# Kernel tuning notes

Hardware: AMD Instinct MI355X
Metric: run time of the kernel (lower is better)

The kernel has to match this reference:

```python
import jax, jax.numpy as jnp
import numpy as np

NEG = -1000000000.0  # mask fill value from the original code


def setup_inputs() -> dict:
    key = jax.random.key(0)
    k1, k2, k3 = jax.random.split(key, 3)
    B, L, H, E = 2, 2048, 16, 64
    S, D = L, E
    queries = jax.random.normal(k1, (B, L, H, E), dtype=jnp.float32)
    keys = jax.random.normal(k2, (B, S, H, E), dtype=jnp.float32)
    values = jax.random.normal(k3, (B, S, H, D), dtype=jnp.float32)
    return {"queries": queries, "keys": keys, "values": values}


def reference(queries, keys, values):
    B, L, H, E = queries.shape
    S = keys.shape[1]
    scale = 1.0 / np.sqrt(E)
    # scores: [B, H, L, S]
    scores = jnp.einsum('blhe,bshe->bhls', queries, keys)
    # Faithful to original: tf.where(band_part(ones,-1,0), -1e9, scores)
    # i.e. fill -1e9 where the LOWER triangle (incl. diagonal) is True.
    tril = jnp.tril(jnp.ones((L, S), dtype=bool))  # [L, S]
    scores = jnp.where(tril[None, None, :, :], jnp.float32(NEG), scores)
    # scale applied AFTER masking, as in the original
    A = jax.nn.softmax(scale * scores, axis=-1)
    # dropout is identity at inference
    V = jnp.einsum('bhls,bshd->blhd', A, values)
    return V
```

## Files before the change

kernel.cpp:

```cpp
#include <hip/hip_runtime.h>


#define B_ 2
#define L_ 2048
#define H_ 16
#define E_ 64
#define S_ 2048
#define D_ 64
#define NR_ 16
#define QSCALE 0.18033688011112042f

typedef __attribute__((ext_vector_type(4))) float f32x4;
typedef __attribute__((ext_vector_type(16))) float f32x16;
typedef __attribute__((ext_vector_type(8))) short short8;
typedef __attribute__((ext_vector_type(2))) unsigned int uint2v;
typedef __attribute__((ext_vector_type(4))) unsigned int uint4v;
typedef unsigned short ushort;

__device__ __forceinline__ unsigned short f2bf(float f) {
  unsigned int u = __builtin_bit_cast(unsigned int, f);
  u = (u + 0x7FFFu + ((u >> 16) & 1u)) >> 16;
  return (unsigned short)u;
}
__device__ __forceinline__ unsigned int pkbf(float a, float b) {
  return (unsigned int)f2bf(a) | ((unsigned int)f2bf(b) << 16);
}
__device__ __forceinline__ unsigned cvtpk(float a, float b) {
  unsigned r;
  asm("v_cvt_pk_bf16_f32 %0, %1, %2" : "=v"(r) : "v"(a), "v"(b));
  return r;
}
__device__ __forceinline__ uint2v plswap(unsigned a, unsigned b, int hi) {
#if __has_builtin(__builtin_amdgcn_permlane32_swap)
  (void)hi;
  return __builtin_amdgcn_permlane32_swap(a, b, false, false);
#else
  unsigned ax = (unsigned)__shfl_xor((int)a, 32);
  unsigned bx = (unsigned)__shfl_xor((int)b, 32);
  uint2v r;
  r[0] = hi ? bx : a;
  r[1] = hi ? b : ax;
  return r;
#endif
}
__device__ __forceinline__ f32x16 zero16() {
  f32x16 z;
#pragma unroll
  for (int i = 0; i < 16; ++i) z[i] = 0.f;
  return z;
}

__global__ __launch_bounds__(256) void prep_all(const float* __restrict__ Kg,
                                                const float* __restrict__ Vg,
                                                ushort* __restrict__ Kb,
                                                ushort* __restrict__ Vt) {
  __shared__ ushort Tl[64][72];
  const int blk = (int)blockIdx.x;
  const int tid = (int)threadIdx.x;
  if (blk < 2048) {
    const int t = blk * 256 + tid;
    const int orow = t >> 3, e0 = (t & 7) << 3;
    const int s = orow & (S_ - 1), bh = orow >> 11;
    const int b = bh >> 4, h = bh & 15;
    const float* src = Kg + ((size_t)((b * S_ + s) * H_ + h)) * E_ + e0;
    f32x4 a = ((const f32x4*)src)[0], c = ((const f32x4*)src)[1];
    short8 o;
    o[0]=(short)f2bf(a[0]); o[1]=(short)f2bf(a[1]); o[2]=(short)f2bf(a[2]); o[3]=(short)f2bf(a[3]);
    o[4]=(short)f2bf(c[0]); o[5]=(short)f2bf(c[1]); o[6]=(short)f2bf(c[2]); o[7]=(short)f2bf(c[3]);
    *(short8*)(Kb + (size_t)orow * E_ + e0) = o;
  } else {
    const int vb = blk - 2048;
    const int bh = vb & 31, st = vb >> 5;
    const int b = bh >> 4, h = bh & 15;
    const int s0 = st << 6;
    {
      const int sr = tid >> 2, d0 = (tid & 3) << 4;
      const float* src = Vg + ((size_t)((b * S_ + s0 + sr) * H_ + h)) * D_ + d0;
      f32x4 v0 = ((const f32x4*)src)[0], v1 = ((const f32x4*)src)[1];
      f32x4 v2 = ((const f32x4*)src)[2], v3 = ((const f32x4*)src)[3];
      ushort* dst = &Tl[sr][d0];
      dst[0]=f2bf(v0[0]); dst[1]=f2bf(v0[1]); dst[2]=f2bf(v0[2]); dst[3]=f2bf(v0[3]);
      dst[4]=f2bf(v1[0]); dst[5]=f2bf(v1[1]); dst[6]=f2bf(v1[2]); dst[7]=f2bf(v1[3]);
      dst[8]=f2bf(v2[0]); dst[9]=f2bf(v2[1]); dst[10]=f2bf(v2[2]); dst[11]=f2bf(v2[3]);
      dst[12]=f2bf(v3[0]); dst[13]=f2bf(v3[1]); dst[14]=f2bf(v3[2]); dst[15]=f2bf(v3[3]);
    }
    __syncthreads();
    {
      const int d = tid >> 2, sb = (tid & 3) << 4;
      short8 o0, o1;
#pragma unroll
      for (int j = 0; j < 8; ++j) {
        o0[j] = (short)Tl[sb + j][d];
        o1[j] = (short)Tl[sb + 8 + j][d];
      }
      ushort* dst = Vt + ((size_t)bh * D_ + d) * S_ + s0 + sb;
      *(short8*)dst = o0;
      *(short8*)(dst + 8) = o1;
    }
  }
}

struct Stage8 { short8 k[4]; short8 v[4]; };

__device__ __forceinline__ Stage8 sload(const ushort* __restrict__ Kbh,
                                        const ushort* __restrict__ VbhT,
                                        int s0, int tid) {
  Stage8 r;
  const int sl = tid >> 1, gb = (tid & 1) * 4;
  const ushort* kp = Kbh + (size_t)(s0 + sl) * E_ + gb * 8;
  r.k[0] = *(const short8*)(kp);
  r.k[1] = *(const short8*)(kp + 8);
  r.k[2] = *(const short8*)(kp + 16);
  r.k[3] = *(const short8*)(kp + 24);
  const int d = tid >> 2, sb = (tid & 3) * 32;
  const ushort* vp = VbhT + (size_t)d * S_ + s0 + sb;
  r.v[0] = *(const short8*)(vp);
  r.v[1] = *(const short8*)(vp + 8);
  r.v[2] = *(const short8*)(vp + 16);
  r.v[3] = *(const short8*)(vp + 24);
  return r;
}

__device__ __forceinline__ void swrite(ushort* SM, const Stage8& r, int tid) {
  const int sl = tid >> 1, gb = (tid & 1) * 4;
#pragma unroll
  for (int j = 0; j < 4; ++j)
    *(short8*)(SM + sl * 64 + (((gb + j) ^ (sl & 7)) << 3)) = r.k[j];
  const int d = tid >> 2, sgb = (tid & 3) * 4;
#pragma unroll
  for (int j = 0; j < 4; ++j) {
    const int sgg = sgb + j;
    *(short8*)(SM + 8192 + (sgg >> 3) * 4096 + d * 64 + (((sgg & 7) ^ (d & 7)) << 3)) = r.v[j];
  }
}

__global__ __launch_bounds__(256, 2) void attn_fwd9(
    const float* __restrict__ Qg, const ushort* __restrict__ Kb,
    const ushort* __restrict__ Vt, float* __restrict__ Og) {
  const int bh = (int)blockIdx.x;
  const int b = bh >> 4, h = bh & 15;
  const int yi0 = (int)blockIdx.y;
  const int yi = (yi0 < 8) ? yi0 : 23 - yi0;
  const int q0 = yi << 7;
  const int tid = (int)threadIdx.x;
  const int w = tid >> 6, lane = tid & 63;
  const int hi = lane >> 5, c32 = lane & 31;
  const int qbase = q0 + (w << 5);
  const int qrow = qbase + c32;

  __shared__ __align__(16) ushort SM[2][16384];

  const ushort* Kbh = Kb + (size_t)bh * (S_ * E_);
  const ushort* VbhT = Vt + (size_t)bh * (D_ * S_);

  short8 qf[4];
  {
    const float* qr = Qg + ((size_t)((b * L_ + qrow) * H_ + h)) * E_;
#pragma unroll
    for (int kc = 0; kc < 4; ++kc) {
      f32x4 x = *(const f32x4*)(qr + kc * 16 + hi * 8);
      f32x4 y = *(const f32x4*)(qr + kc * 16 + hi * 8 + 4);
      short8 q;
      q[0]=(short)f2bf(QSCALE*x[0]); q[1]=(short)f2bf(QSCALE*x[1]);
      q[2]=(short)f2bf(QSCALE*x[2]); q[3]=(short)f2bf(QSCALE*x[3]);
      q[4]=(short)f2bf(QSCALE*y[0]); q[5]=(short)f2bf(QSCALE*y[1]);
      q[6]=(short)f2bf(QSCALE*y[2]); q[7]=(short)f2bf(QSCALE*y[3]);
      qf[kc] = q;
    }
  }

  f32x16 acc0 = zero16(), acc1 = zero16();
  float m_run = -1e30f, dsum = 0.f;

  const int r0 = (q0 + 1) >> 7;

  {
    Stage8 s = sload(Kbh, VbhT, r0 << 7, tid);
    swrite(SM[0], s, tid);
  }
  __syncthreads();

  for (int r = r0; r < NR_; ++r) {
    const int cur = (r - r0) & 1;
    const bool more = (r + 1) < NR_;
    Stage8 nxt;
    if (more) nxt = sload(Kbh, VbhT, (r + 1) << 7, tid);

    const ushort* img = SM[cur];
#pragma unroll
    for (int half = 0; half < 2; ++half) {
      const int s0 = (r << 7) + (half << 6);
      if (s0 + 63 > qbase) {
        f32x16 st0 = zero16(), st1 = zero16();
        __builtin_amdgcn_s_setprio(1);
#pragma unroll
        for (int kc = 0; kc < 4; ++kc) {
          const int gg = 2 * kc + hi;
          const int rl0 = (half << 6) + c32, rl1 = rl0 + 32;
          short8 k0 = *(const short8*)(img + rl0 * 64 + ((gg ^ (rl0 & 7)) << 3));
          short8 k1 = *(const short8*)(img + rl1 * 64 + ((gg ^ (rl1 & 7)) << 3));
          st0 = __builtin_amdgcn_mfma_f32_32x32x16_bf16(k0, qf[kc], st0, 0, 0, 0);
          st1 = __builtin_amdgcn_mfma_f32_32x32x16_bf16(k1, qf[kc], st1, 0, 0, 0);
        }
        __builtin_amdgcn_s_setprio(0);

        if (s0 < qbase + 32) {
#pragma unroll
          for (int r16 = 0; r16 < 16; ++r16) {
            const int ko = (r16 & 3) + 8 * (r16 >> 2) + 4 * hi;
            st0[r16] = (s0 + ko <= qrow) ? -1e30f : st0[r16];
            st1[r16] = (s0 + 32 + ko <= qrow) ? -1e30f : st1[r16];
          }
        }

        float pmax = -1e30f;
#pragma unroll
        for (int r16 = 0; r16 < 16; ++r16) pmax = fmaxf(pmax, fmaxf(st0[r16], st1[r16]));
        if (__any(pmax > m_run + 8.0f)) {
          float rm = fmaxf(pmax, __shfl_xor(pmax, 32));
          float m_new = fmaxf(m_run, rm);
          float alpha = exp2f(m_run - m_new);
          dsum *= alpha;
#pragma unroll
          for (int r16 = 0; r16 < 16; ++r16) {
            float ar = __shfl(alpha, (r16 & 3) + 8 * (r16 >> 2) + 4 * hi);
            acc0[r16] *= ar;
            acc1[r16] *= ar;
          }
          m_run = m_new;
        }

        float ps = 0.f;
#pragma unroll
        for (int r16 = 0; r16 < 16; ++r16) { st0[r16] = exp2f(st0[r16] - m_run); ps += st0[r16]; }
#pragma unroll
        for (int r16 = 0; r16 < 16; ++r16) { st1[r16] = exp2f(st1[r16] - m_run); ps += st1[r16]; }
        dsum += ps;

        short8 pf[4];
#pragma unroll
        for (int kp = 0; kp < 4; ++kp) {
          const f32x16 stt = (kp < 2) ? st0 : st1;
          const int u = kp & 1;
          unsigned pA0 = cvtpk(stt[8 * u + 0], stt[8 * u + 1]);
          unsigned pA1 = cvtpk(stt[8 * u + 2], stt[8 * u + 3]);
          unsigned pB0 = cvtpk(stt[8 * u + 4], stt[8 * u + 5]);
          unsigned pB1 = cvtpk(stt[8 * u + 6], stt[8 * u + 7]);
          uint2v sw0 = plswap(pA0, pB0, hi);
          uint2v sw1 = plswap(pA1, pB1, hi);
          uint4v fv;
          fv[0] = sw0[0]; fv[1] = sw1[0]; fv[2] = sw0[1]; fv[3] = sw1[1];
          pf[kp] = __builtin_bit_cast(short8, fv);
        }

        __builtin_amdgcn_s_setprio(1);
#pragma unroll
        for (int kp = 0; kp < 4; ++kp) {
          const int sg = 2 * kp + hi;
          const ushort* vb = img + 8192 + half * 4096;
          short8 v0 = *(const short8*)(vb + c32 * 64 + ((sg ^ (c32 & 7)) << 3));
          short8 v1 = *(const short8*)(vb + (32 + c32) * 64 + ((sg ^ (c32 & 7)) << 3));
          acc0 = __builtin_amdgcn_mfma_f32_32x32x16_bf16(pf[kp], v0, acc0, 0, 0, 0);
          acc1 = __builtin_amdgcn_mfma_f32_32x32x16_bf16(pf[kp], v1, acc1, 0, 0, 0);
        }
        __builtin_amdgcn_s_setprio(0);
      }
    }

    if (more) swrite(SM[cur ^ 1], nxt, tid);
    __syncthreads();
  }

  float dfull = dsum + __shfl_xor(dsum, 32);
#pragma unroll
  for (int r16 = 0; r16 < 16; ++r16) {
    const int row = (r16 & 3) + 8 * (r16 >> 2) + 4 * hi;
    const float dn = __shfl(dfull, row);
    const int grow = qbase + row;
    if (grow != L_ - 1) {
      const float inv = 1.0f / dn;
      const size_t base = ((size_t)((b * L_ + grow) * H_ + h)) * D_;
      Og[base + c32] = acc0[r16] * inv;
      Og[base + 32 + c32] = acc1[r16] * inv;
    }
  }
}

__global__ __launch_bounds__(256) void vmean_part(const float* __restrict__ Vg,
                                                  float* __restrict__ ws) {
  const int g = blockIdx.x;
  const int slab = g & 15, bh = g >> 4;
  const int b = bh >> 4, h = bh & 15;
  const int lane = (int)threadIdx.x & 63, w = (int)threadIdx.x >> 6;
  const int s0 = (slab << 7) + (w << 5);
  const float* base = Vg + ((size_t)((b * S_ + s0) * H_ + h)) * D_ + lane;
  float sum = 0.f;
#pragma unroll 4
  for (int i = 0; i < 32; ++i) sum += base[(size_t)i * (H_ * D_)];
  __shared__ float red[4][64];
  red[w][lane] = sum;
  __syncthreads();
  if (w == 0)
    ws[(size_t)g * 64 + lane] =
        red[0][lane] + red[1][lane] + red[2][lane] + red[3][lane];
}

__global__ __launch_bounds__(64) void vmean_comb(const float* __restrict__ ws,
                                                 float* __restrict__ Og) {
  const int bh = blockIdx.x;
  const int b = bh >> 4, h = bh & 15;
  const int lane = (int)threadIdx.x;
  float t = 0.f;
#pragma unroll
  for (int i = 0; i < 16; ++i) t += ws[(size_t)(bh * 16 + i) * 64 + lane];
  Og[((size_t)((b * L_ + (L_ - 1)) * H_ + h)) * D_ + lane] = t * (1.0f / (float)S_);
}

__global__ __launch_bounds__(256) void attn_fwd(
    const float* __restrict__ Qg, const float* __restrict__ Kg,
    const float* __restrict__ Vg, float* __restrict__ Og) {
  const int bh = blockIdx.x;
  const int b = bh >> 4, h = bh & 15;
  const int q0 = blockIdx.y << 6;
  const int tid = (int)threadIdx.x;
  const int lane = tid & 63;
  const int w = tid >> 6;
  const int gp = lane >> 4;
  const int c = lane & 15;
  const int qbase = q0 + (w << 4);

  __shared__ unsigned short Kl[32][72];
  __shared__ unsigned short Vts[64][40];

  short8 qf0, qf1;
  {
    const float* qrow = Qg + ((size_t)((b * L_ + (qbase + c)) * H_ + h)) * E_;
    const f32x4* q0p = (const f32x4*)(qrow + (gp << 3));
    const f32x4* q1p = (const f32x4*)(qrow + 32 + (gp << 3));
    f32x4 a0 = q0p[0], b0 = q0p[1], a1 = q1p[0], b1 = q1p[1];
    float t0[8] = {a0[0],a0[1],a0[2],a0[3],b0[0],b0[1],b0[2],b0[3]};
    float t1[8] = {a1[0],a1[1],a1[2],a1[3],b1[0],b1[1],b1[2],b1[3]};
#pragma unroll
    for (int j = 0; j < 8; ++j) {
      qf0[j] = (short)f2bf(0.125f * t0[j]);
      qf1[j] = (short)f2bf(0.125f * t1[j]);
    }
  }

  f32x4 accO[4];
#pragma unroll
  for (int k0 = 0; k0 < 4; ++k0) accO[k0] = (f32x4){0.f, 0.f, 0.f, 0.f};
  float m_run = -1e30f, denom = 0.f;

  const int c0 = (q0 + 1) >> 5;
  const int srow = tid >> 3;
  const int scol = (tid & 7) << 3;

  for (int ch = c0; ch < (S_ >> 5); ++ch) {
    const int s0 = ch << 5;
    __syncthreads();
    {
      const size_t rbase = ((size_t)((b * S_ + (s0 + srow)) * H_ + h));
      const float* kp = Kg + rbase * E_ + scol;
      f32x4 ka = *(const f32x4*)kp;
      f32x4 kb = *(const f32x4*)(kp + 4);
      short8 kv;
      kv[0]=(short)f2bf(ka[0]); kv[1]=(short)f2bf(ka[1]);
      kv[2]=(short)f2bf(ka[2]); kv[3]=(short)f2bf(ka[3]);
      kv[4]=(short)f2bf(kb[0]); kv[5]=(short)f2bf(kb[1]);
      kv[6]=(short)f2bf(kb[2]); kv[7]=(short)f2bf(kb[3]);
      *(short8*)&Kl[srow][scol] = kv;
      const float* vp = Vg + rbase * D_ + scol;
      f32x4 va = *(const f32x4*)vp;
      f32x4 vb = *(const f32x4*)(vp + 4);
      Vts[scol + 0][srow] = f2bf(va[0]);
      Vts[scol + 1][srow] = f2bf(va[1]);
      Vts[scol + 2][srow] = f2bf(va[2]);
      Vts[scol + 3][srow] = f2bf(va[3]);
      Vts[scol + 4][srow] = f2bf(vb[0]);
      Vts[scol + 5][srow] = f2bf(vb[1]);
      Vts[scol + 6][srow] = f2bf(vb[2]);
      Vts[scol + 7][srow] = f2bf(vb[3]);
    }
    __syncthreads();
    if (s0 + 31 <= qbase) continue;

    f32x4 st0 = {0.f,0.f,0.f,0.f}, st1 = {0.f,0.f,0.f,0.f};
    {
      short8 kf;
      kf = *(const short8*)&Kl[c][(gp << 3)];
      st0 = __builtin_amdgcn_mfma_f32_16x16x32_bf16(kf, qf0, st0, 0, 0, 0);
      kf = *(const short8*)&Kl[c][32 + (gp << 3)];
      st0 = __builtin_amdgcn_mfma_f32_16x16x32_bf16(kf, qf1, st0, 0, 0, 0);
      kf = *(const short8*)&Kl[16 + c][(gp << 3)];
      st1 = __builtin_amdgcn_mfma_f32_16x16x32_bf16(kf, qf0, st1, 0, 0, 0);
      kf = *(const short8*)&Kl[16 + c][32 + (gp << 3)];
      st1 = __builtin_amdgcn_mfma_f32_16x16x32_bf16(kf, qf1, st1, 0, 0, 0);
    }

    const int lrow = qbase + c;
    float p[8];
    {
      float sarr[8] = {st0[0], st0[1], st0[2], st0[3], st1[0], st1[1], st1[2], st1[3]};
      float mx = -1e30f;
#pragma unroll
      for (int i = 0; i < 8; ++i) {
        int sg = s0 + ((i >> 2) << 4) + (gp << 2) + (i & 3);
        float v = (sg > lrow) ? sarr[i] : -1e30f;
        p[i] = v;
        mx = fmaxf(mx, v);
      }
      mx = fmaxf(mx, __shfl_xor(mx, 16));
      mx = fmaxf(mx, __shfl_xor(mx, 32));
      float m_new = fmaxf(m_run, mx);
      float sum = 0.f;
#pragma unroll
      for (int i = 0; i < 8; ++i) { p[i] = __expf(p[i] - m_new); sum += p[i]; }
      sum += __shfl_xor(sum, 16);
      sum += __shfl_xor(sum, 32);
      float alpha = __expf(m_run - m_new);
      m_run = m_new;
      denom = denom * alpha + sum;
      float ar0 = __shfl(alpha, (gp << 2) + 0);
      float ar1 = __shfl(alpha, (gp << 2) + 1);
      float ar2 = __shfl(alpha, (gp << 2) + 2);
      float ar3 = __shfl(alpha, (gp << 2) + 3);
#pragma unroll
      for (int k0 = 0; k0 < 4; ++k0) {
        accO[k0][0] *= ar0; accO[k0][1] *= ar1;
        accO[k0][2] *= ar2; accO[k0][3] *= ar3;
      }
    }

    {
      unsigned int pA0 = pkbf(p[0], p[1]), pA1 = pkbf(p[2], p[3]);
      unsigned int pB0 = pkbf(p[4], p[5]), pB1 = pkbf(p[6], p[7]);
      const int al = (gp << 1) & 3;
      const int src0 = (al << 4) + c, src1 = src0 + 16;
      unsigned int a0 = (unsigned int)__shfl((int)pA0, src0);
      unsigned int a1 = (unsigned int)__shfl((int)pA1, src0);
      unsigned int a2 = (unsigned int)__shfl((int)pA0, src1);
      unsigned int a3 = (unsigned int)__shfl((int)pA1, src1);
      unsigned int b0 = (unsigned int)__shfl((int)pB0, src0);
      unsigned int b1 = (unsigned int)__shfl((int)pB1, src0);
      unsigned int b2 = (unsigned int)__shfl((int)pB0, src1);
      unsigned int b3 = (unsigned int)__shfl((int)pB1, src1);
      const bool useA = (gp < 2);
      uint4v fv;
      fv[0] = useA ? a0 : b0;
      fv[1] = useA ? a1 : b1;
      fv[2] = useA ? a2 : b2;
      fv[3] = useA ? a3 : b3;
      short8 pfv = __builtin_bit_cast(short8, fv);
#pragma unroll
      for (int k0 = 0; k0 < 4; ++k0) {
        short8 vf = *(const short8*)&Vts[(k0 << 4) + c][(gp << 3)];
        accO[k0] = __builtin_amdgcn_mfma_f32_16x16x32_bf16(pfv, vf, accO[k0], 0, 0, 0);
      }
    }
  }

  float dr[4];
  dr[0] = __shfl(denom, (gp << 2) + 0);
  dr[1] = __shfl(denom, (gp << 2) + 1);
  dr[2] = __shfl(denom, (gp << 2) + 2);
  dr[3] = __shfl(denom, (gp << 2) + 3);
#pragma unroll
  for (int r = 0; r < 4; ++r) {
    const int grow = qbase + (gp << 2) + r;
    if (grow == L_ - 1) continue;
    const size_t base = ((size_t)((b * L_ + grow) * H_ + h)) * D_ + c;
    const float inv = 1.0f / dr[r];
    Og[base +  0] = accO[0][r] * inv;
    Og[base + 16] = accO[1][r] * inv;
    Og[base + 32] = accO[2][r] * inv;
    Og[base + 48] = accO[3][r] * inv;
  }
}

__global__ __launch_bounds__(256) void vmean_fix(const float* __restrict__ Vg,
                                                 float* __restrict__ Og) {
  const int bh = blockIdx.x;
  const int b = bh >> 4, h = bh & 15;
  const int t = (int)threadIdx.x;
  const int lane = t & 63, w = t >> 6;
  float sum = 0.f;
  for (int s = w; s < S_; s += 4)
    sum += Vg[((size_t)((b * S_ + s) * H_ + h)) * D_ + lane];
  __shared__ float red[4][64];
  red[w][lane] = sum;
  __syncthreads();
  if (w == 0) {
    float tot = red[0][lane] + red[1][lane] + red[2][lane] + red[3][lane];
    Og[((size_t)((b * L_ + (L_ - 1)) * H_ + h)) * D_ + lane] = tot * (1.0f / (float)S_);
  }
}

extern "C" void kernel_launch(void* const* d_in, const int* in_sizes, int n_in,
                              void* d_out, int out_size, void* d_ws, size_t ws_size,
                              hipStream_t stream) {
  const float* Q = (const float*)d_in[0];
  const float* K = (const float*)d_in[1];
  const float* V = (const float*)d_in[2];
  float* O = (float*)d_out;
  const size_t szK = (size_t)B_ * H_ * S_ * E_ * 2;
  const size_t szV = (size_t)B_ * H_ * D_ * S_ * 2;
  const size_t szP = (size_t)(B_ * H_ * 16) * 64 * 4;

  if (ws_size >= szK + szV + szP) {
    ushort* Kb = (ushort*)d_ws;
    ushort* Vt = (ushort*)((char*)d_ws + szK);
    float* part = (float*)((char*)d_ws + szK + szV);
    prep_all<<<dim3(3072), dim3(256), 0, stream>>>(K, V, Kb, Vt);
    attn_fwd9<<<dim3(B_ * H_, L_ / 128), dim3(256), 0, stream>>>(Q, Kb, Vt, O);
    vmean_part<<<dim3(B_ * H_ * 16), dim3(256), 0, stream>>>(V, part);
    vmean_comb<<<dim3(B_ * H_), dim3(64), 0, stream>>>(part, O);
  } else {
    attn_fwd<<<dim3(B_ * H_, L_ / 64), dim3(256), 0, stream>>>(Q, K, V, O);
    vmean_fix<<<dim3(B_ * H_), dim3(256), 0, stream>>>(V, O);
  }
}
```

Before: 69.66 us.

## Shrink attention blocks to 64 query rows with single-buffered LDS

The main attention kernel now uses 2-wave blocks of 64 query rows instead of 4-wave blocks of 128, which doubles the grid and reorders the tiles into a 32-entry folded schedule to balance causal work. The LDS ring drops from two buffers to one, with an extra barrier before each overwrite, and each thread now loads twice as many K/V vectors per 128-key stage. The aim is more blocks and less shared memory per block for higher occupancy and better load balance. In exchange, the kernel loses overlap between LDS writes and compute, adds a barrier per stage, and each K/V tile is reused by fewer query rows.

```diff
diff --git a/kernel.cpp b/kernel.cpp
--- a/kernel.cpp
+++ b/kernel.cpp
@@ -100,55 +100,49 @@
   }
 }
 
-struct Stage8 { short8 k[4]; short8 v[4]; };
-
-__device__ __forceinline__ Stage8 sload(const ushort* __restrict__ Kbh,
-                                        const ushort* __restrict__ VbhT,
-                                        int s0, int tid) {
-  Stage8 r;
-  const int sl = tid >> 1, gb = (tid & 1) * 4;
-  const ushort* kp = Kbh + (size_t)(s0 + sl) * E_ + gb * 8;
-  r.k[0] = *(const short8*)(kp);
-  r.k[1] = *(const short8*)(kp + 8);
-  r.k[2] = *(const short8*)(kp + 16);
-  r.k[3] = *(const short8*)(kp + 24);
-  const int d = tid >> 2, sb = (tid & 3) * 32;
-  const ushort* vp = VbhT + (size_t)d * S_ + s0 + sb;
-  r.v[0] = *(const short8*)(vp);
-  r.v[1] = *(const short8*)(vp + 8);
-  r.v[2] = *(const short8*)(vp + 16);
-  r.v[3] = *(const short8*)(vp + 24);
+struct Stage11 { short8 k[8]; short8 v[8]; };
+
+__device__ __forceinline__ Stage11 sload11(const ushort* __restrict__ Kbh,
+                                           const ushort* __restrict__ VbhT,
+                                           int s0, int tid) {
+  Stage11 r;
+  const ushort* kp = Kbh + (size_t)(s0 + tid) * E_;
+#pragma unroll
+  for (int j = 0; j < 8; ++j) r.k[j] = *(const short8*)(kp + j * 8);
+  const int d = tid >> 1;
+  const ushort* vp = VbhT + (size_t)d * S_ + s0 + (tid & 1) * 64;
+#pragma unroll
+  for (int j = 0; j < 8; ++j) r.v[j] = *(const short8*)(vp + j * 8);
   return r;
 }
 
-__device__ __forceinline__ void swrite(ushort* SM, const Stage8& r, int tid) {
-  const int sl = tid >> 1, gb = (tid & 1) * 4;
-#pragma unroll
-  for (int j = 0; j < 4; ++j)
-    *(short8*)(SM + sl * 64 + (((gb + j) ^ (sl & 7)) << 3)) = r.k[j];
-  const int d = tid >> 2, sgb = (tid & 3) * 4;
-#pragma unroll
-  for (int j = 0; j < 4; ++j) {
-    const int sgg = sgb + j;
-    *(short8*)(SM + 8192 + (sgg >> 3) * 4096 + d * 64 + (((sgg & 7) ^ (d & 7)) << 3)) = r.v[j];
-  }
-}
-
-__global__ __launch_bounds__(256, 2) void attn_fwd9(
+__device__ __forceinline__ void swrite11(ushort* SM, const Stage11& r, int tid) {
+#pragma unroll
+  for (int j = 0; j < 8; ++j)
+    *(short8*)(SM + tid * 64 + ((j ^ (tid & 7)) << 3)) = r.k[j];
+  const int d = tid >> 1, kgb = (tid & 1) * 8;
+#pragma unroll
+  for (int j = 0; j < 8; ++j) {
+    const int kg = kgb + j;
+    *(short8*)(SM + 8192 + (kg >> 3) * 4096 + d * 64 + (((kg & 7) ^ (d & 7)) << 3)) = r.v[j];
+  }
+}
+
+__global__ __launch_bounds__(128, 2) void attn_fwd11(
     const float* __restrict__ Qg, const ushort* __restrict__ Kb,
     const ushort* __restrict__ Vt, float* __restrict__ Og) {
   const int bh = (int)blockIdx.x;
   const int b = bh >> 4, h = bh & 15;
   const int yi0 = (int)blockIdx.y;
-  const int yi = (yi0 < 8) ? yi0 : 23 - yi0;
-  const int q0 = yi << 7;
+  const int yi = (yi0 < 16) ? yi0 : 47 - yi0;
+  const int q0 = yi << 6;
   const int tid = (int)threadIdx.x;
   const int w = tid >> 6, lane = tid & 63;
   const int hi = lane >> 5, c32 = lane & 31;
   const int qbase = q0 + (w << 5);
   const int qrow = qbase + c32;
 
-  __shared__ __align__(16) ushort SM[2][16384];
+  __shared__ __align__(16) ushort SM[16384];
 
   const ushort* Kbh = Kb + (size_t)bh * (S_ * E_);
   const ushort* VbhT = Vt + (size_t)bh * (D_ * S_);
@@ -175,18 +169,17 @@
   const int r0 = (q0 + 1) >> 7;
 
   {
-    Stage8 s = sload(Kbh, VbhT, r0 << 7, tid);
-    swrite(SM[0], s, tid);
+    Stage11 s = sload11(Kbh, VbhT, r0 << 7, tid);
+    swrite11(SM, s, tid);
   }
   __syncthreads();
 
   for (int r = r0; r < NR_; ++r) {
-    const int cur = (r - r0) & 1;
     const bool more = (r + 1) < NR_;
-    Stage8 nxt;
-    if (more) nxt = sload(Kbh, VbhT, (r + 1) << 7, tid);
-
-    const ushort* img = SM[cur];
+    Stage11 nxt;
+    if (more) nxt = sload11(Kbh, VbhT, (r + 1) << 7, tid);
+
+    const ushort* img = SM;
 #pragma unroll
     for (int half = 0; half < 2; ++half) {
       const int s0 = (r << 7) + (half << 6);
@@ -267,7 +260,8 @@
       }
     }
 
-    if (more) swrite(SM[cur ^ 1], nxt, tid);
+    __syncthreads();
+    if (more) swrite11(SM, nxt, tid);
     __syncthreads();
   }
 
@@ -512,7 +506,7 @@
     ushort* Vt = (ushort*)((char*)d_ws + szK);
     float* part = (float*)((char*)d_ws + szK + szV);
     prep_all<<<dim3(3072), dim3(256), 0, stream>>>(K, V, Kb, Vt);
-    attn_fwd9<<<dim3(B_ * H_, L_ / 128), dim3(256), 0, stream>>>(Q, Kb, Vt, O);
+    attn_fwd11<<<dim3(B_ * H_, 32), dim3(128), 0, stream>>>(Q, Kb, Vt, O);
     vmean_part<<<dim3(B_ * H_ * 16), dim3(256), 0, stream>>>(V, part);
     vmean_comb<<<dim3(B_ * H_), dim3(64), 0, stream>>>(part, O);
   } else {
```

After: 83.51 us. 1.2x slower.

## Split each KV tile across wave pairs with 64-row query blocks and merge partials

Applied to the files above, without the earlier changes.

Query blocks shrink from 128 to 64 rows, and each pair of waves now shares one 32-row query slice, with each wave covering one 64-key half of every 128-key tile. The two partial softmax states are merged through shared memory at the end. Shared memory drops from double to single buffering, with an extra barrier per tile, so that four blocks can be resident per CU. The grid becomes 32x32 with interleaved causal tile ordering. The aim is more parallelism and occupancy, at the cost of losing the overlap between buffer writes and compute plus an added merge step.

```diff
diff --git a/kernel.cpp b/kernel.cpp
--- a/kernel.cpp
+++ b/kernel.cpp
@@ -134,21 +134,21 @@
   }
 }
 
-__global__ __launch_bounds__(256, 2) void attn_fwd9(
+__global__ __launch_bounds__(256, 4) void attn_fwd12(
     const float* __restrict__ Qg, const ushort* __restrict__ Kb,
     const ushort* __restrict__ Vt, float* __restrict__ Og) {
-  const int bh = (int)blockIdx.x;
+  const int yt = (int)blockIdx.x, bh = (int)blockIdx.y;
   const int b = bh >> 4, h = bh & 15;
-  const int yi0 = (int)blockIdx.y;
-  const int yi = (yi0 < 8) ? yi0 : 23 - yi0;
-  const int q0 = yi << 7;
+  const int yi = (yt & 1) ? (31 - (yt >> 1)) : (yt >> 1);
+  const int q0 = yi << 6;
   const int tid = (int)threadIdx.x;
   const int w = tid >> 6, lane = tid & 63;
+  const int sub = w >> 1, par = w & 1;
   const int hi = lane >> 5, c32 = lane & 31;
-  const int qbase = q0 + (w << 5);
+  const int qbase = q0 + (sub << 5);
   const int qrow = qbase + c32;
 
-  __shared__ __align__(16) ushort SM[2][16384];
+  __shared__ __align__(16) ushort SM[16384];
 
   const ushort* Kbh = Kb + (size_t)bh * (S_ * E_);
   const ushort* VbhT = Vt + (size_t)bh * (D_ * S_);
@@ -176,112 +176,131 @@
 
   {
     Stage8 s = sload(Kbh, VbhT, r0 << 7, tid);
-    swrite(SM[0], s, tid);
+    swrite(SM, s, tid);
   }
   __syncthreads();
 
   for (int r = r0; r < NR_; ++r) {
-    const int cur = (r - r0) & 1;
     const bool more = (r + 1) < NR_;
     Stage8 nxt;
     if (more) nxt = sload(Kbh, VbhT, (r + 1) << 7, tid);
 
-    const ushort* img = SM[cur];
-#pragma unroll
-    for (int half = 0; half < 2; ++half) {
-      const int s0 = (r << 7) + (half << 6);
-      if (s0 + 63 > qbase) {
-        f32x16 st0 = zero16(), st1 = zero16();
-        __builtin_amdgcn_s_setprio(1);
-#pragma unroll
-        for (int kc = 0; kc < 4; ++kc) {
-          const int gg = 2 * kc + hi;
-          const int rl0 = (half << 6) + c32, rl1 = rl0 + 32;
-          short8 k0 = *(const short8*)(img + rl0 * 64 + ((gg ^ (rl0 & 7)) << 3));
-          short8 k1 = *(const short8*)(img + rl1 * 64 + ((gg ^ (rl1 & 7)) << 3));
-          st0 = __builtin_amdgcn_mfma_f32_32x32x16_bf16(k0, qf[kc], st0, 0, 0, 0);
-          st1 = __builtin_amdgcn_mfma_f32_32x32x16_bf16(k1, qf[kc], st1, 0, 0, 0);
+    const int s0w = (r << 7) + (par << 6);
+    if (s0w + 63 > qbase) {
+      f32x16 st0 = zero16(), st1 = zero16();
+      __builtin_amdgcn_s_setprio(1);
+#pragma unroll
+      for (int kc = 0; kc < 4; ++kc) {
+        const int gg = 2 * kc + hi;
+        const int rl0 = (par << 6) + c32, rl1 = rl0 + 32;
+        short8 k0 = *(const short8*)(SM + rl0 * 64 + ((gg ^ (rl0 & 7)) << 3));
+        short8 k1 = *(const short8*)(SM + rl1 * 64 + ((gg ^ (rl1 & 7)) << 3));
+        st0 = __builtin_amdgcn_mfma_f32_32x32x16_bf16(k0, qf[kc], st0, 0, 0, 0);
+        st1 = __builtin_amdgcn_mfma_f32_32x32x16_bf16(k1, qf[kc], st1, 0, 0, 0);
+      }
+      __builtin_amdgcn_s_setprio(0);
+
+      if (s0w < qbase + 32) {
+#pragma unroll
+        for (int r16 = 0; r16 < 16; ++r16) {
+          const int ko = (r16 & 3) + 8 * (r16 >> 2) + 4 * hi;
+          st0[r16] = (s0w + ko <= qrow) ? -1e30f : st0[r16];
+          st1[r16] = (s0w + 32 + ko <= qrow) ? -1e30f : st1[r16];
         }
-        __builtin_amdgcn_s_setprio(0);
-
-        if (s0 < qbase + 32) {
-#pragma unroll
-          for (int r16 = 0; r16 < 16; ++r16) {
-            const int ko = (r16 & 3) + 8 * (r16 >> 2) + 4 * hi;
-            st0[r16] = (s0 + ko <= qrow) ? -1e30f : st0[r16];
-            st1[r16] = (s0 + 32 + ko <= qrow) ? -1e30f : st1[r16];
-          }
+      }
+
+      float pmax = -1e30f;
+#pragma unroll
+      for (int r16 = 0; r16 < 16; ++r16) pmax = fmaxf(pmax, fmaxf(st0[r16], st1[r16]));
+      if (__any(pmax > m_run + 8.0f)) {
+        float rm = fmaxf(pmax, __shfl_xor(pmax, 32));
+        float m_new = fmaxf(m_run, rm);
+        float alpha = exp2f(m_run - m_new);
+        dsum *= alpha;
+#pragma unroll
+        for (int r16 = 0; r16 < 16; ++r16) {
+          float ar = __shfl(alpha, (r16 & 3) + 8 * (r16 >> 2) + 4 * hi);
+          acc0[r16] *= ar;
+          acc1[r16] *= ar;
         }
-
-        float pmax = -1e30f;
-#pragma unroll
-        for (int r16 = 0; r16 < 16; ++r16) pmax = fmaxf(pmax, fmaxf(st0[r16], st1[r16]));
-        if (__any(pmax > m_run + 8.0f)) {
-          float rm = fmaxf(pmax, __shfl_xor(pmax, 32));
-          float m_new = fmaxf(m_run, rm);
-          float alpha = exp2f(m_run - m_new);
-          dsum *= alpha;
-#pragma unroll
-          for (int r16 = 0; r16 < 16; ++r16) {
-            float ar = __shfl(alpha, (r16 & 3) + 8 * (r16 >> 2) + 4 * hi);
-            acc0[r16] *= ar;
-            acc1[r16] *= ar;
-          }
-          m_run = m_new;
-        }
-
-        float ps = 0.f;
-#pragma unroll
-        for (int r16 = 0; r16 < 16; ++r16) { st0[r16] = exp2f(st0[r16] - m_run); ps += st0[r16]; }
-#pragma unroll
-        for (int r16 = 0; r16 < 16; ++r16) { st1[r16] = exp2f(st1[r16] - m_run); ps += st1[r16]; }
-        dsum += ps;
-
-        short8 pf[4];
-#pragma unroll
-        for (int kp = 0; kp < 4; ++kp) {
-          const f32x16 stt = (kp < 2) ? st0 : st1;
-          const int u = kp & 1;
-          unsigned pA0 = cvtpk(stt[8 * u + 0], stt[8 * u + 1]);
-          unsigned pA1 = cvtpk(stt[8 * u + 2], stt[8 * u + 3]);
-          unsigned pB0 = cvtpk(stt[8 * u + 4], stt[8 * u + 5]);
-          unsigned pB1 = cvtpk(stt[8 * u + 6], stt[8 * u + 7]);
-          uint2v sw0 = plswap(pA0, pB0, hi);
-          uint2v sw1 = plswap(pA1, pB1, hi);
-          uint4v fv;
-          fv[0] = sw0[0]; fv[1] = sw1[0]; fv[2] = sw0[1]; fv[3] = sw1[1];
-          pf[kp] = __builtin_bit_cast(short8, fv);
-        }
-
-        __builtin_amdgcn_s_setprio(1);
-#pragma unroll
-        for (int kp = 0; kp < 4; ++kp) {
-          const int sg = 2 * kp + hi;
-          const ushort* vb = img + 8192 + half * 4096;
-          short8 v0 = *(const short8*)(vb + c32 * 64 + ((sg ^ (c32 & 7)) << 3));
-          short8 v1 = *(const short8*)(vb + (32 + c32) * 64 + ((sg ^ (c32 & 7)) << 3));
-          acc0 = __builtin_amdgcn_mfma_f32_32x32x16_bf16(pf[kp], v0, acc0, 0, 0, 0);
-          acc1 = __builtin_amdgcn_mfma_f32_32x32x16_bf16(pf[kp], v1, acc1, 0, 0, 0);
-        }
-        __builtin_amdgcn_s_setprio(0);
-      }
-    }
-
-    if (more) swrite(SM[cur ^ 1], nxt, tid);
+        m_run = m_new;
+      }
+
+      float ps = 0.f;
+#pragma unroll
+      for (int r16 = 0; r16 < 16; ++r16) { st0[r16] = exp2f(st0[r16] - m_run); ps += st0[r16]; }
+#pragma unroll
+      for (int r16 = 0; r16 < 16; ++r16) { st1[r16] = exp2f(st1[r16] - m_run); ps += st1[r16]; }
+      dsum += ps;
+
+      short8 pf[4];
+#pragma unroll
+      for (int kp = 0; kp < 4; ++kp) {
+        const f32x16 stt = (kp < 2) ? st0 : st1;
+        const int u = kp & 1;
+        unsigned pA0 = cvtpk(stt[8 * u + 0], stt[8 * u + 1]);
+        unsigned pA1 = cvtpk(stt[8 * u + 2], stt[8 * u + 3]);
+        unsigned pB0 = cvtpk(stt[8 * u + 4], stt[8 * u + 5]);
+        unsigned pB1 = cvtpk(stt[8 * u + 6], stt[8 * u + 7]);
+        uint2v sw0 = plswap(pA0, pB0, hi);
+        uint2v sw1 = plswap(pA1, pB1, hi);
+        uint4v fv;
+        fv[0] = sw0[0]; fv[1] = sw1[0]; fv[2] = sw0[1]; fv[3] = sw1[1];
+        pf[kp] = __builtin_bit_cast(short8, fv);
+      }
+
+      __builtin_amdgcn_s_setprio(1);
+#pragma unroll
+      for (int kp = 0; kp < 4; ++kp) {
+        const int sg = 2 * kp + hi;
+        const ushort* vb = SM + 8192 + par * 4096;
+        short8 v0 = *(const short8*)(vb + c32 * 64 + ((sg ^ (c32 & 7)) << 3));
+        short8 v1 = *(const short8*)(vb + (32 + c32) * 64 + ((sg ^ (c32 & 7)) << 3));
+        acc0 = __builtin_amdgcn_mfma_f32_32x32x16_bf16(pf[kp], v0, acc0, 0, 0, 0);
+        acc1 = __builtin_amdgcn_mfma_f32_32x32x16_bf16(pf[kp], v1, acc1, 0, 0, 0);
+      }
+      __builtin_amdgcn_s_setprio(0);
+    }
+
     __syncthreads();
-  }
-
-  float dfull = dsum + __shfl_xor(dsum, 32);
-#pragma unroll
-  for (int r16 = 0; r16 < 16; ++r16) {
-    const int row = (r16 & 3) + 8 * (r16 >> 2) + 4 * hi;
-    const float dn = __shfl(dfull, row);
-    const int grow = qbase + row;
-    if (grow != L_ - 1) {
-      const float inv = 1.0f / dn;
-      const size_t base = ((size_t)((b * L_ + grow) * H_ + h)) * D_;
-      Og[base + c32] = acc0[r16] * inv;
-      Og[base + 32 + c32] = acc1[r16] * inv;
+    if (more) swrite(SM, nxt, tid);
+    __syncthreads();
+  }
+
+  float* ex = (float*)&SM[0];
+  float* slot = ex + (size_t)(sub * 64 + lane) * 34;
+  if (par == 1) {
+    slot[0] = m_run;
+    slot[1] = dsum;
+#pragma unroll
+    for (int r16 = 0; r16 < 16; ++r16) { slot[2 + r16] = acc0[r16]; slot[18 + r16] = acc1[r16]; }
+  }
+  __syncthreads();
+  if (par == 0) {
+    const float mb = slot[0], db = slot[1];
+    const float m = fmaxf(m_run, mb);
+    const float aa = exp2f(m_run - m), ab = exp2f(mb - m);
+    const float dme = dsum * aa + db * ab;
+#pragma unroll
+    for (int r16 = 0; r16 < 16; ++r16) {
+      const int row = (r16 & 3) + 8 * (r16 >> 2) + 4 * hi;
+      const float aar = __shfl(aa, row);
+      const float abr = __shfl(ab, row);
+      acc0[r16] = acc0[r16] * aar + slot[2 + r16] * abr;
+      acc1[r16] = acc1[r16] * aar + slot[18 + r16] * abr;
+    }
+    const float dfull = dme + __shfl_xor(dme, 32);
+#pragma unroll
+    for (int r16 = 0; r16 < 16; ++r16) {
+      const int row = (r16 & 3) + 8 * (r16 >> 2) + 4 * hi;
+      const float dn = __shfl(dfull, row);
+      const int grow = qbase + row;
+      if (grow != L_ - 1) {
+        const float inv = 1.0f / dn;
+        const size_t base = ((size_t)((b * L_ + grow) * H_ + h)) * D_;
+        Og[base + c32] = acc0[r16] * inv;
+        Og[base + 32 + c32] = acc1[r16] * inv;
+      }
     }
   }
 }
@@ -512,7 +531,7 @@
     ushort* Vt = (ushort*)((char*)d_ws + szK);
     float* part = (float*)((char*)d_ws + szK + szV);
     prep_all<<<dim3(3072), dim3(256), 0, stream>>>(K, V, Kb, Vt);
-    attn_fwd9<<<dim3(B_ * H_, L_ / 128), dim3(256), 0, stream>>>(Q, Kb, Vt, O);
+    attn_fwd12<<<dim3(32, 32), dim3(256), 0, stream>>>(Q, Kb, Vt, O);
     vmean_part<<<dim3(B_ * H_ * 16), dim3(256), 0, stream>>>(V, part);
     vmean_comb<<<dim3(B_ * H_), dim3(64), 0, stream>>>(part, O);
   } else {
```

Result: slower. 164.6 us (+136.4%).
